# Optimization experiments

Hardware: AMD Instinct MI355X
Metric: run time of the kernel (lower is better)

The kernel has to match this reference:

```python
import jax, jax.numpy as jnp
import numpy as np

E = 1024      # embed_dim
H = 16        # n_heads
B = 8         # number of varlen segments
LQ = 512      # query tokens per segment (uniform packing)
LKV = 1024    # kv tokens per segment (uniform packing)


def setup_inputs() -> dict:
    key = jax.random.key(0)
    k0, k1, k2, k3 = jax.random.split(key, 4)
    inputs = jax.random.normal(k0, (B * LKV, E), dtype=jnp.float32)
    queries = jax.random.normal(k1, (B * LQ, E), dtype=jnp.float32)
    # cu_seqlens: prefix sums of segment lengths (uniform segments here)
    cu_seqlens_inputs = jnp.arange(B + 1, dtype=jnp.int32) * LKV
    cu_seqlens_queries = jnp.arange(B + 1, dtype=jnp.int32) * LQ
    # nn.MultiheadAttention parameters
    scale = 0.02
    w_in = jax.random.normal(k2, (3 * E, E), dtype=jnp.float32) * scale
    b_in = jnp.zeros((3 * E,), dtype=jnp.float32)
    w_out = jax.random.normal(k3, (E, E), dtype=jnp.float32) * scale
    b_out = jnp.zeros((E,), dtype=jnp.float32)
    return {
        "inputs": inputs,
        "queries": queries,
        "w_in": w_in,
        "b_in": b_in,
        "w_out": w_out,
        "b_out": b_out,
        "cu_seqlens_inputs": cu_seqlens_inputs,
        "cu_seqlens_queries": cu_seqlens_queries,
    }


def reference(inputs, queries, w_in, b_in, w_out, b_out,
              cu_seqlens_inputs, cu_seqlens_queries):
    # Packed varlen cross-attention. Segments are uniform (as produced by
    # setup_inputs), so the ragged computation is expressed as a single
    # batched attention: reshape packed tokens to [B, L, E]. Attention is
    # confined within each segment, matching the original per-segment loop.
    e = inputs.shape[-1]
    dh = e // H
    b = cu_seqlens_inputs.shape[0] - 1
    lkv = inputs.shape[0] // b
    lq = queries.shape[0] // b

    # in_proj: torch computes x @ W.T + b with W = in_proj_weight rows [q;k;v]
    q = queries @ w_in[:e].T + b_in[:e]
    k = inputs @ w_in[e:2 * e].T + b_in[e:2 * e]
    v = inputs @ w_in[2 * e:].T + b_in[2 * e:]

    q = q.reshape(b, lq, H, dh)
    k = k.reshape(b, lkv, H, dh)
    v = v.reshape(b, lkv, H, dh)

    scale = 1.0 / jnp.sqrt(jnp.asarray(dh, q.dtype))
    scores = jnp.einsum('bqhd,bkhd->bhqk', q, k) * scale   # [B,H,Lq,Lkv]
    probs = jax.nn.softmax(scores, axis=-1)
    o = jnp.einsum('bhqk,bkhd->bqhd', probs, v).reshape(b * lq, e)
    return o @ w_out.T + b_out
```

## Files before the change

kernel.cpp:

```cpp
#include <hip/hip_runtime.h>

#define E_DIM 1024
#define NH 16
#define DH 64
#define BSEG 8
#define LQ 512
#define LKV 1024

typedef short bf16x8 __attribute__((ext_vector_type(8)));
typedef float f32x4 __attribute__((ext_vector_type(4)));
typedef unsigned short u16;

__device__ __forceinline__ u16 f2bf(float x) {
    unsigned u = __float_as_uint(x);
    u += 0x7FFF + ((u >> 16) & 1);
    return (u16)(u >> 16);
}

__device__ __forceinline__ void async16(const void* g, const void* l) {
    __builtin_amdgcn_global_load_lds(
        (const __attribute__((address_space(1))) unsigned int*)g,
        (__attribute__((address_space(3))) unsigned int*)l, 16, 0, 0);
}

__device__ __forceinline__ unsigned pk2(float a, float b) {
    unsigned r;
    asm("v_cvt_pk_bf16_f32 %0, %1, %2" : "=v"(r) : "v"(a), "v"(b));
    return r;
}

__global__ __launch_bounds__(256) void cvt_all_kernel(
    const float* __restrict__ inputs, const float* __restrict__ queries,
    const float* __restrict__ w_in, const float* __restrict__ w_out,
    u16* __restrict__ ib, u16* __restrict__ qb,
    u16* __restrict__ wib, u16* __restrict__ wob)
{
    int blk = blockIdx.x;
    const float* s; u16* d; int base;
    if (blk < 8192)        { s = inputs;  d = ib;  base = blk; }
    else if (blk < 12288)  { s = queries; d = qb;  base = blk - 8192; }
    else if (blk < 15360)  { s = w_in;    d = wib; base = blk - 12288; }
    else                   { s = w_out;   d = wob; base = blk - 15360; }
    int i = base * 256 + threadIdx.x;
    float4 v = ((const float4*)s)[i];
    ushort4 o;
    o.x = f2bf(v.x); o.y = f2bf(v.y); o.z = f2bf(v.z); o.w = f2bf(v.w);
    ((ushort4*)d)[i] = o;
}

__global__ __launch_bounds__(256, 5) void proj_gemm_kernel(
    const u16* __restrict__ inputs_b, const u16* __restrict__ queries_b,
    const u16* __restrict__ w_in_b, const float* __restrict__ b_in,
    u16* __restrict__ Kf, u16* __restrict__ Qf, u16* __restrict__ Vf)
{
    __shared__ u16 As[2][128 * 32];
    __shared__ u16 Ws[2][128 * 32];

    const int bid = blockIdx.x;
    const bool isQ = (bid >= 1024);
    const int x = bid & 7;
    int bx, by;
    if (!isQ) { int i = bid >> 3;          bx = i >> 3; by = x * 8 + (i & 7); }
    else      { int i = (bid - 1024) >> 3; bx = i >> 2; by = x * 4 + (i & 3); }

    const u16* A = isQ ? queries_b : inputs_b;
    const u16* W = w_in_b + (isQ ? 0 : (size_t)E_DIM * E_DIM);
    const float* bias = b_in + (isQ ? 0 : E_DIM);
    const int m_blk = by * 128;
    const int n_blk = bx * 128;
    const int K = E_DIM;

    const int tid = threadIdx.x;
    const int l = tid & 63;
    const int w = tid >> 6;
    const int m0 = (w & 1) * 64;
    const int n0 = (w >> 1) * 64;
    const int quad = l >> 4;
    const int c = l & 15;

    f32x4 acc[4][4];
    #pragma unroll
    for (int i = 0; i < 4; ++i)
        #pragma unroll
        for (int j = 0; j < 4; ++j)
            acc[i][j] = (f32x4){0.f, 0.f, 0.f, 0.f};

    const int srow = l >> 2;
    const int skoff = (l & 3) * 8;
    const u16* Ag = A + (size_t)(m_blk + w * 32 + srow) * K + skoff;
    const u16* Wg = W + (size_t)(n_blk + w * 32 + srow) * K + skoff;

    for (int k0 = 0; k0 < K; k0 += 64) {
        __syncthreads();
        #pragma unroll
        for (int hf = 0; hf < 2; ++hf)
            #pragma unroll
            for (int t = 0; t < 2; ++t) {
                const size_t soff = (size_t)t * 16 * K + k0 + hf * 32;
                const size_t doff = (size_t)(w * 32 + t * 16) * 32;
                async16(Ag + soff, &As[hf][0] + doff);
                async16(Wg + soff, &Ws[hf][0] + doff);
            }
        __syncthreads();

        #pragma unroll
        for (int hf = 0; hf < 2; ++hf) {
            bf16x8 af[4], wf[4];
            #pragma unroll
            for (int t = 0; t < 4; ++t) {
                af[t] = *(const bf16x8*)&As[hf][(m0 + t * 16 + c) * 32 + quad * 8];
                wf[t] = *(const bf16x8*)&Ws[hf][(n0 + t * 16 + c) * 32 + quad * 8];
            }
            #pragma unroll
            for (int i = 0; i < 4; ++i)
                #pragma unroll
                for (int j = 0; j < 4; ++j)
                    acc[i][j] = __builtin_amdgcn_mfma_f32_16x16x32_bf16(
                        af[i], wf[j], acc[i][j], 0, 0, 0);
        }
    }

    #pragma unroll
    for (int jj = 0; jj < 4; ++jj) {
        int col = n_blk + n0 + jj * 16 + c;
        float bv = bias[col];
        if (isQ || col < 1024) {
            u16* dst = isQ ? Qf : Kf;
            int hh = col >> 6, d = col & 63;
            int dq = d >> 3, dj = d & 7;
            #pragma unroll
            for (int i = 0; i < 4; ++i) {
                int t = (m_blk + m0 + i * 16) >> 4;
                size_t base = ((size_t)(t * NH + hh)) * 1024
                            + (size_t)(dq * 16 + quad * 4) * 8 + dj;
                #pragma unroll
                for (int r = 0; r < 4; ++r)
                    dst[base + (size_t)r * 8] = f2bf(acc[i][jj][r] + bv);
            }
        } else {
            int vcol = col - 1024;
            int hv = vcol >> 6, d = vcol & 63;
            int td = d >> 4, ct = d & 15;
            #pragma unroll
            for (int i = 0; i < 4; ++i) {
                int tok = m_blk + m0 + i * 16;
                int g32 = tok >> 5;
                int jo = (tok & 16) >> 2;
                ushort4 pk;
                pk.x = f2bf(acc[i][jj][0] + bv);
                pk.y = f2bf(acc[i][jj][1] + bv);
                pk.z = f2bf(acc[i][jj][2] + bv);
                pk.w = f2bf(acc[i][jj][3] + bv);
                *(ushort4*)(Vf + ((size_t)(g32 * NH + hv)) * 2048
                            + (size_t)((td * 4 + quad) * 16 + ct) * 8 + jo) = pk;
            }
        }
    }
}

__global__ __launch_bounds__(256) void attn_kernel(
    const u16* __restrict__ Qf, const u16* __restrict__ Kf,
    const u16* __restrict__ Vf, u16* __restrict__ Ob)
{
    __shared__ u16 Ks[2][4096];
    __shared__ u16 Vs[2][4096];

    const int tid = threadIdx.x;
    const int l = tid & 63;
    const int w = tid >> 6;
    const int quad = l >> 4;
    const int c = l & 15;
    const int bid = blockIdx.x;
    const int h = bid & 15;
    const int b = (bid >> 4) & 7;
    const int qt = bid >> 7;
    const int q0 = b * LQ + qt * 64 + w * 16;
    const float C1 = 0.18033688011112042f;
    const float THR = 8.0f;

    bf16x8 qf[2];
    {
        size_t qb = ((size_t)((q0 >> 4) * NH + h)) * 1024 + (size_t)l * 8;
        qf[0] = *(const bf16x8*)(Qf + qb);
        qf[1] = *(const bf16x8*)(Qf + qb + 512);
    }

    f32x4 o[4];
    #pragma unroll
    for (int td = 0; td < 4; ++td) o[td] = (f32x4){0.f, 0.f, 0.f, 0.f};
    float m_i = -1e30f;
    float lpart = 0.f;

    auto stage = [&](int buf, int kv0) {
        const int kvg = b * LKV + kv0;
        const int t16 = kvg >> 4;
        const int t32 = kvg >> 5;
        #pragma unroll
        for (int r = 0; r < 2; ++r) {
            const int nt = 2 * r + (w >> 1);
            const u16* ksrc = Kf + ((size_t)((t16 + nt) * NH + h)) * 1024
                            + (w & 1) * 512 + l * 8;
            async16(ksrc, &Ks[buf][r * 2048 + w * 512 + l * 8]);
            const u16* vsrc = Vf + ((size_t)((t32 + r) * NH + h)) * 2048
                            + w * 512 + l * 8;
            async16(vsrc, &Vs[buf][r * 2048 + w * 512 + l * 8]);
        }
    };

    auto step_lds = [&](int buf) {
        f32x4 s[4];
        #pragma unroll
        for (int nt = 0; nt < 4; ++nt) s[nt] = (f32x4){0.f, 0.f, 0.f, 0.f};
        __builtin_amdgcn_s_setprio(1);
        #pragma unroll
        for (int nt = 0; nt < 4; ++nt)
            #pragma unroll
            for (int hk = 0; hk < 2; ++hk) {
                bf16x8 kf = *(const bf16x8*)&Ks[buf][nt * 1024 + hk * 512 + l * 8];
                s[nt] = __builtin_amdgcn_mfma_f32_16x16x32_bf16(
                    kf, qf[hk], s[nt], 0, 0, 0);
            }
        __builtin_amdgcn_s_setprio(0);

        float m01 = fmaxf(fmaxf(s[0][0], s[0][1]), fmaxf(s[0][2], s[0][3]));
        float m23 = fmaxf(fmaxf(s[1][0], s[1][1]), fmaxf(s[1][2], s[1][3]));
        float m45 = fmaxf(fmaxf(s[2][0], s[2][1]), fmaxf(s[2][2], s[2][3]));
        float m67 = fmaxf(fmaxf(s[3][0], s[3][1]), fmaxf(s[3][2], s[3][3]));
        float vml = fmaxf(fmaxf(m01, m23), fmaxf(m45, m67));

        if (!__all(vml - m_i <= THR)) {
            float vmr = vml;
            vmr = fmaxf(vmr, __shfl_xor(vmr, 16, 64));
            vmr = fmaxf(vmr, __shfl_xor(vmr, 32, 64));
            float mnew = fmaxf(m_i, vmr);
            float alpha = __builtin_amdgcn_exp2f((m_i - mnew) * C1);
            m_i = mnew;
            lpart *= alpha;
            float ar[4];
            #pragma unroll
            for (int r = 0; r < 4; ++r) ar[r] = __shfl(alpha, quad * 4 + r, 16);
            #pragma unroll
            for (int td = 0; td < 4; ++td)
                #pragma unroll
                for (int r = 0; r < 4; ++r) o[td][r] *= ar[r];
        }

        float p[4][4];
        float rs = 0.f;
        #pragma unroll
        for (int nt = 0; nt < 4; ++nt)
            #pragma unroll
            for (int r = 0; r < 4; ++r) {
                p[nt][r] = __builtin_amdgcn_exp2f((s[nt][r] - m_i) * C1);
                rs += p[nt][r];
            }
        lpart += rs;

        bf16x8 af[2];
        #pragma unroll
        for (int g = 0; g < 2; ++g) {
            union { unsigned u[4]; bf16x8 v; } r_;
            r_.u[0] = pk2(p[2 * g][0],     p[2 * g][1]);
            r_.u[1] = pk2(p[2 * g][2],     p[2 * g][3]);
            r_.u[2] = pk2(p[2 * g + 1][0], p[2 * g + 1][1]);
            r_.u[3] = pk2(p[2 * g + 1][2], p[2 * g + 1][3]);
            af[g] = r_.v;
        }

        __builtin_amdgcn_s_setprio(1);
        #pragma unroll
        for (int g = 0; g < 2; ++g)
            #pragma unroll
            for (int td = 0; td < 4; ++td) {
                bf16x8 vf = *(const bf16x8*)&Vs[buf][g * 2048 + td * 512 + l * 8];
                o[td] = __builtin_amdgcn_mfma_f32_16x16x32_bf16(
                    af[g], vf, o[td], 0, 0, 0);
            }
        __builtin_amdgcn_s_setprio(0);
    };

    stage(0, 0);
    __syncthreads();
    int cur = 0;
    #pragma unroll 2
    for (int it = 0; it < 16; ++it) {
        if (it < 15) stage(cur ^ 1, (it + 1) * 64);
        step_lds(cur);
        __syncthreads();
        cur ^= 1;
    }

    float l_i = lpart;
    l_i += __shfl_xor(l_i, 16, 64);
    l_i += __shfl_xor(l_i, 32, 64);
    float invl = 1.f / l_i;
    float ir[4];
    #pragma unroll
    for (int r = 0; r < 4; ++r) ir[r] = __shfl(invl, quad * 4 + r, 16);
    #pragma unroll
    for (int td = 0; td < 4; ++td)
        #pragma unroll
        for (int r = 0; r < 4; ++r)
            Ob[(size_t)(q0 + quad * 4 + r) * E_DIM + h * 64 + td * 16 + c] =
                f2bf(o[td][r] * ir[r]);
}

__global__ __launch_bounds__(256) void out_gemm_kernel(
    const u16* __restrict__ A, const u16* __restrict__ W,
    const float* __restrict__ bias, float* __restrict__ Cf)
{
    __shared__ u16 As[2][64 * 32];
    __shared__ u16 Ws[2][64 * 32];

    const int K = E_DIM, N = E_DIM;
    const int bid = blockIdx.x;
    const int x = bid & 7;
    const int i_ = bid >> 3;
    const int m_blk = (x * 8 + (i_ & 7)) * 64;
    const int n_blk = (i_ >> 3) * 64;

    const int tid = threadIdx.x;
    const int l = tid & 63;
    const int w = tid >> 6;
    const int m0 = (w & 1) * 32;
    const int n0 = (w >> 1) * 32;
    const int quad = l >> 4;
    const int c = l & 15;

    f32x4 acc[2][2];
    #pragma unroll
    for (int i = 0; i < 2; ++i)
        #pragma unroll
        for (int j = 0; j < 2; ++j)
            acc[i][j] = (f32x4){0.f, 0.f, 0.f, 0.f};

    const int srow = l >> 2;
    const int skoff = (l & 3) * 8;
    const u16* Ag = A + (size_t)(m_blk + w * 16 + srow) * K + skoff;
    const u16* Wg = W + (size_t)(n_blk + w * 16 + srow) * K + skoff;

    for (int k0 = 0; k0 < K; k0 += 64) {
        __syncthreads();
        #pragma unroll
        for (int hf = 0; hf < 2; ++hf) {
            const size_t soff = (size_t)(k0 + hf * 32);
            const size_t doff = (size_t)(w * 16) * 32;
            async16(Ag + soff, &As[hf][0] + doff);
            async16(Wg + soff, &Ws[hf][0] + doff);
        }
        __syncthreads();

        #pragma unroll
        for (int hf = 0; hf < 2; ++hf) {
            bf16x8 af[2], wf[2];
            #pragma unroll
            for (int t = 0; t < 2; ++t) {
                af[t] = *(const bf16x8*)&As[hf][(m0 + t * 16 + c) * 32 + quad * 8];
                wf[t] = *(const bf16x8*)&Ws[hf][(n0 + t * 16 + c) * 32 + quad * 8];
            }
            #pragma unroll
            for (int i = 0; i < 2; ++i)
                #pragma unroll
                for (int j = 0; j < 2; ++j)
                    acc[i][j] = __builtin_amdgcn_mfma_f32_16x16x32_bf16(
                        wf[j], af[i], acc[i][j], 0, 0, 0);
        }
    }

    #pragma unroll
    for (int j = 0; j < 2; ++j) {
        const int colb = n_blk + n0 + j * 16 + quad * 4;
        const float4 bv = *(const float4*)&bias[colb];
        #pragma unroll
        for (int i = 0; i < 2; ++i) {
            const int row = m_blk + m0 + i * 16 + c;
            float4 o4;
            o4.x = acc[i][j][0] + bv.x;
            o4.y = acc[i][j][1] + bv.y;
            o4.z = acc[i][j][2] + bv.z;
            o4.w = acc[i][j][3] + bv.w;
            *(float4*)&Cf[(size_t)row * N + colb] = o4;
        }
    }
}

extern "C" void kernel_launch(void* const* d_in, const int* in_sizes, int n_in,
                              void* d_out, int out_size, void* d_ws, size_t ws_size,
                              hipStream_t stream) {
    const float* inputs  = (const float*)d_in[0];
    const float* queries = (const float*)d_in[1];
    const float* w_in    = (const float*)d_in[2];
    const float* b_in    = (const float*)d_in[3];
    const float* w_out   = (const float*)d_in[4];
    const float* b_out   = (const float*)d_in[5];
    float* out = (float*)d_out;

    const int NQ = BSEG * LQ;
    const int NKV = BSEG * LKV;

    u16* inputs_b  = (u16*)d_ws;
    u16* queries_b = inputs_b  + (size_t)NKV * E_DIM;
    u16* w_in_b    = queries_b + (size_t)NQ * E_DIM;
    u16* w_out_b   = w_in_b    + (size_t)3 * E_DIM * E_DIM;
    u16* Qf        = w_out_b   + (size_t)E_DIM * E_DIM;
    u16* Kf        = Qf        + (size_t)NQ * E_DIM;
    u16* Vf        = Kf        + (size_t)NKV * E_DIM;
    u16* Ob        = Vf        + (size_t)NKV * E_DIM;

    dim3 blk(256);

    cvt_all_kernel<<<16384, blk, 0, stream>>>(
        inputs, queries, w_in, w_out, inputs_b, queries_b, w_in_b, w_out_b);

    proj_gemm_kernel<<<1280, blk, 0, stream>>>(
        inputs_b, queries_b, w_in_b, b_in, Kf, Qf, Vf);

    attn_kernel<<<1024, blk, 0, stream>>>(Qf, Kf, Vf, Ob);

    out_gemm_kernel<<<1024, blk, 0, stream>>>(
        Ob, w_out_b, b_out, out);
}
```

Before: 215.1 us.

## Fuse fp32-to-bf16 activation conversion into projection GEMM A-tile loads

The standalone conversion of inputs and queries to bf16 is dropped. The projection GEMM now loads fp32 activation tiles into registers, one K-step ahead, packs them to bf16 and writes them to shared memory, while weights still use async global-to-LDS loads. This removes a full read-write pass over about 12M activation elements and one set of workspace buffers. In exchange the GEMM reads twice as many A bytes per tile and holds more registers, which could lower occupancy under the launch bound of 5.

```diff
diff --git a/kernel.cpp b/kernel.cpp
--- a/kernel.cpp
+++ b/kernel.cpp
@@ -29,18 +29,23 @@
     return r;
 }
 
-__global__ __launch_bounds__(256) void cvt_all_kernel(
-    const float* __restrict__ inputs, const float* __restrict__ queries,
+__device__ __forceinline__ bf16x8 pk8(f32x4 lo, f32x4 hi) {
+    union { unsigned u[4]; bf16x8 v; } r;
+    r.u[0] = pk2(lo[0], lo[1]);
+    r.u[1] = pk2(lo[2], lo[3]);
+    r.u[2] = pk2(hi[0], hi[1]);
+    r.u[3] = pk2(hi[2], hi[3]);
+    return r.v;
+}
+
+__global__ __launch_bounds__(256) void cvt_w_kernel(
     const float* __restrict__ w_in, const float* __restrict__ w_out,
-    u16* __restrict__ ib, u16* __restrict__ qb,
     u16* __restrict__ wib, u16* __restrict__ wob)
 {
     int blk = blockIdx.x;
     const float* s; u16* d; int base;
-    if (blk < 8192)        { s = inputs;  d = ib;  base = blk; }
-    else if (blk < 12288)  { s = queries; d = qb;  base = blk - 8192; }
-    else if (blk < 15360)  { s = w_in;    d = wib; base = blk - 12288; }
-    else                   { s = w_out;   d = wob; base = blk - 15360; }
+    if (blk < 3072) { s = w_in;  d = wib; base = blk; }
+    else            { s = w_out; d = wob; base = blk - 3072; }
     int i = base * 256 + threadIdx.x;
     float4 v = ((const float4*)s)[i];
     ushort4 o;
@@ -49,7 +54,7 @@
 }
 
 __global__ __launch_bounds__(256, 5) void proj_gemm_kernel(
-    const u16* __restrict__ inputs_b, const u16* __restrict__ queries_b,
+    const float* __restrict__ inputs, const float* __restrict__ queries,
     const u16* __restrict__ w_in_b, const float* __restrict__ b_in,
     u16* __restrict__ Kf, u16* __restrict__ Qf, u16* __restrict__ Vf)
 {
@@ -63,7 +68,7 @@
     if (!isQ) { int i = bid >> 3;          bx = i >> 3; by = x * 8 + (i & 7); }
     else      { int i = (bid - 1024) >> 3; bx = i >> 2; by = x * 4 + (i & 3); }
 
-    const u16* A = isQ ? queries_b : inputs_b;
+    const float* A = isQ ? queries : inputs;
     const u16* W = w_in_b + (isQ ? 0 : (size_t)E_DIM * E_DIM);
     const float* bias = b_in + (isQ ? 0 : E_DIM);
     const int m_blk = by * 128;
@@ -87,9 +92,32 @@
 
     const int srow = l >> 2;
     const int skoff = (l & 3) * 8;
-    const u16* Ag = A + (size_t)(m_blk + w * 32 + srow) * K + skoff;
-    const u16* Wg = W + (size_t)(n_blk + w * 32 + srow) * K + skoff;
-
+    const float* Ag = A + (size_t)(m_blk + w * 32 + srow) * K + skoff;
+    const u16*   Wg = W + (size_t)(n_blk + w * 32 + srow) * K + skoff;
+
+    f32x4 ar[8];
+    auto loadA = [&](int k0) {
+        #pragma unroll
+        for (int hf = 0; hf < 2; ++hf)
+            #pragma unroll
+            for (int t = 0; t < 2; ++t) {
+                const float* p = Ag + (size_t)t * 16 * K + k0 + hf * 32;
+                ar[(hf * 2 + t) * 2 + 0] = *(const f32x4*)p;
+                ar[(hf * 2 + t) * 2 + 1] = *(const f32x4*)(p + 4);
+            }
+    };
+    auto writeA = [&]() {
+        #pragma unroll
+        for (int hf = 0; hf < 2; ++hf)
+            #pragma unroll
+            for (int t = 0; t < 2; ++t) {
+                bf16x8 pk = pk8(ar[(hf * 2 + t) * 2 + 0],
+                                ar[(hf * 2 + t) * 2 + 1]);
+                *(bf16x8*)&As[hf][(size_t)(w * 32 + t * 16) * 32 + l * 8] = pk;
+            }
+    };
+
+    loadA(0);
     for (int k0 = 0; k0 < K; k0 += 64) {
         __syncthreads();
         #pragma unroll
@@ -98,10 +126,11 @@
             for (int t = 0; t < 2; ++t) {
                 const size_t soff = (size_t)t * 16 * K + k0 + hf * 32;
                 const size_t doff = (size_t)(w * 32 + t * 16) * 32;
-                async16(Ag + soff, &As[hf][0] + doff);
                 async16(Wg + soff, &Ws[hf][0] + doff);
             }
+        writeA();
         __syncthreads();
+        if (k0 + 64 < K) loadA(k0 + 64);
 
         #pragma unroll
         for (int hf = 0; hf < 2; ++hf) {
@@ -236,13 +265,13 @@
             float alpha = __builtin_amdgcn_exp2f((m_i - mnew) * C1);
             m_i = mnew;
             lpart *= alpha;
-            float ar[4];
-            #pragma unroll
-            for (int r = 0; r < 4; ++r) ar[r] = __shfl(alpha, quad * 4 + r, 16);
+            float ar_[4];
+            #pragma unroll
+            for (int r = 0; r < 4; ++r) ar_[r] = __shfl(alpha, quad * 4 + r, 16);
             #pragma unroll
             for (int td = 0; td < 4; ++td)
                 #pragma unroll
-                for (int r = 0; r < 4; ++r) o[td][r] *= ar[r];
+                for (int r = 0; r < 4; ++r) o[td][r] *= ar_[r];
         }
 
         float p[4][4];
@@ -398,22 +427,20 @@
     const int NQ = BSEG * LQ;
     const int NKV = BSEG * LKV;
 
-    u16* inputs_b  = (u16*)d_ws;
-    u16* queries_b = inputs_b  + (size_t)NKV * E_DIM;
-    u16* w_in_b    = queries_b + (size_t)NQ * E_DIM;
-    u16* w_out_b   = w_in_b    + (size_t)3 * E_DIM * E_DIM;
-    u16* Qf        = w_out_b   + (size_t)E_DIM * E_DIM;
-    u16* Kf        = Qf        + (size_t)NQ * E_DIM;
-    u16* Vf        = Kf        + (size_t)NKV * E_DIM;
-    u16* Ob        = Vf        + (size_t)NKV * E_DIM;
+    u16* w_in_b  = (u16*)d_ws;
+    u16* w_out_b = w_in_b  + (size_t)3 * E_DIM * E_DIM;
+    u16* Qf      = w_out_b + (size_t)E_DIM * E_DIM;
+    u16* Kf      = Qf      + (size_t)NQ * E_DIM;
+    u16* Vf      = Kf      + (size_t)NKV * E_DIM;
+    u16* Ob      = Vf      + (size_t)NKV * E_DIM;
 
     dim3 blk(256);
 
-    cvt_all_kernel<<<16384, blk, 0, stream>>>(
-        inputs, queries, w_in, w_out, inputs_b, queries_b, w_in_b, w_out_b);
+    cvt_w_kernel<<<4096, blk, 0, stream>>>(
+        w_in, w_out, w_in_b, w_out_b);
 
     proj_gemm_kernel<<<1280, blk, 0, stream>>>(
-        inputs_b, queries_b, w_in_b, b_in, Kf, Qf, Vf);
+        inputs, queries, w_in_b, b_in, Kf, Qf, Vf);
 
     attn_kernel<<<1024, blk, 0, stream>>>(Qf, Kf, Vf, Ob);
 
```

Result: slower. 532.1 us (+147.4%).

## Software-pipeline attention so QK of next tile overlaps softmax/PV of previous

Applied to the files above, without the earlier changes.

The attention loop is split into a QK-score stage and a softmax-plus-PV stage. Scores for tile t are computed while tile t-1 goes through softmax and PV, so MFMA work can overlap the exp/shuffle-heavy softmax. V gets a third LDS buffer because V tiles now stay live one iteration longer. The loop is fully unrolled, which adds a second score register set and raises register pressure and code size.

```diff
diff --git a/kernel.cpp b/kernel.cpp
--- a/kernel.cpp
+++ b/kernel.cpp
@@ -163,7 +163,7 @@
     const u16* __restrict__ Vf, u16* __restrict__ Ob)
 {
     __shared__ u16 Ks[2][4096];
-    __shared__ u16 Vs[2][4096];
+    __shared__ u16 Vs[3][4096];
 
     const int tid = threadIdx.x;
     const int l = tid & 63;
@@ -191,7 +191,7 @@
     float m_i = -1e30f;
     float lpart = 0.f;
 
-    auto stage = [&](int buf, int kv0) {
+    auto stage = [&](int kb, int vb, int kv0) {
         const int kvg = b * LKV + kv0;
         const int t16 = kvg >> 4;
         const int t32 = kvg >> 5;
@@ -200,15 +200,14 @@
             const int nt = 2 * r + (w >> 1);
             const u16* ksrc = Kf + ((size_t)((t16 + nt) * NH + h)) * 1024
                             + (w & 1) * 512 + l * 8;
-            async16(ksrc, &Ks[buf][r * 2048 + w * 512 + l * 8]);
+            async16(ksrc, &Ks[kb][r * 2048 + w * 512 + l * 8]);
             const u16* vsrc = Vf + ((size_t)((t32 + r) * NH + h)) * 2048
                             + w * 512 + l * 8;
-            async16(vsrc, &Vs[buf][r * 2048 + w * 512 + l * 8]);
+            async16(vsrc, &Vs[vb][r * 2048 + w * 512 + l * 8]);
         }
     };
 
-    auto step_lds = [&](int buf) {
-        f32x4 s[4];
+    auto qk = [&](const u16* Kbuf, f32x4* s) {
         #pragma unroll
         for (int nt = 0; nt < 4; ++nt) s[nt] = (f32x4){0.f, 0.f, 0.f, 0.f};
         __builtin_amdgcn_s_setprio(1);
@@ -216,12 +215,14 @@
         for (int nt = 0; nt < 4; ++nt)
             #pragma unroll
             for (int hk = 0; hk < 2; ++hk) {
-                bf16x8 kf = *(const bf16x8*)&Ks[buf][nt * 1024 + hk * 512 + l * 8];
+                bf16x8 kf = *(const bf16x8*)&Kbuf[nt * 1024 + hk * 512 + l * 8];
                 s[nt] = __builtin_amdgcn_mfma_f32_16x16x32_bf16(
                     kf, qf[hk], s[nt], 0, 0, 0);
             }
         __builtin_amdgcn_s_setprio(0);
-
+    };
+
+    auto smpv = [&](f32x4* s, const u16* Vbuf) {
         float m01 = fmaxf(fmaxf(s[0][0], s[0][1]), fmaxf(s[0][2], s[0][3]));
         float m23 = fmaxf(fmaxf(s[1][0], s[1][1]), fmaxf(s[1][2], s[1][3]));
         float m45 = fmaxf(fmaxf(s[2][0], s[2][1]), fmaxf(s[2][2], s[2][3]));
@@ -236,13 +237,13 @@
             float alpha = __builtin_amdgcn_exp2f((m_i - mnew) * C1);
             m_i = mnew;
             lpart *= alpha;
-            float ar[4];
-            #pragma unroll
-            for (int r = 0; r < 4; ++r) ar[r] = __shfl(alpha, quad * 4 + r, 16);
+            float ar_[4];
+            #pragma unroll
+            for (int r = 0; r < 4; ++r) ar_[r] = __shfl(alpha, quad * 4 + r, 16);
             #pragma unroll
             for (int td = 0; td < 4; ++td)
                 #pragma unroll
-                for (int r = 0; r < 4; ++r) o[td][r] *= ar[r];
+                for (int r = 0; r < 4; ++r) o[td][r] *= ar_[r];
         }
 
         float p[4][4];
@@ -272,23 +273,26 @@
         for (int g = 0; g < 2; ++g)
             #pragma unroll
             for (int td = 0; td < 4; ++td) {
-                bf16x8 vf = *(const bf16x8*)&Vs[buf][g * 2048 + td * 512 + l * 8];
+                bf16x8 vf = *(const bf16x8*)&Vbuf[g * 2048 + td * 512 + l * 8];
                 o[td] = __builtin_amdgcn_mfma_f32_16x16x32_bf16(
                     af[g], vf, o[td], 0, 0, 0);
             }
         __builtin_amdgcn_s_setprio(0);
     };
 
-    stage(0, 0);
+    f32x4 sA[4], sB[4];
+    stage(0, 0, 0);
     __syncthreads();
-    int cur = 0;
-    #pragma unroll 2
-    for (int it = 0; it < 16; ++it) {
-        if (it < 15) stage(cur ^ 1, (it + 1) * 64);
-        step_lds(cur);
+    stage(1, 1, 64);
+    qk(Ks[0], sA);
+    #pragma unroll
+    for (int t = 1; t < 16; ++t) {
         __syncthreads();
-        cur ^= 1;
-    }
+        if (t < 15) stage((t + 1) & 1, (t + 1) % 3, (t + 1) * 64);
+        if (t & 1) { qk(Ks[1], sB); smpv(sA, Vs[(t - 1) % 3]); }
+        else       { qk(Ks[0], sA); smpv(sB, Vs[(t - 1) % 3]); }
+    }
+    smpv(sB, Vs[0]);
 
     float l_i = lpart;
     l_i += __shfl_xor(l_i, 16, 64);
```

Result: no change. 216.8 us (+0.8%).
